# Kernel tuning notes

Measured on AMD Instinct MI355X. Metric: run time of the kernel, lower is better.

The kernel has to match this reference:

```python
import jax, jax.numpy as jnp
import numpy as np

N_NODES = 50000
N_EDGES = 800000
IN_F = 256
HID = 128
OUT_F = 128
HEADS = 4
NEG_SLOPE = 0.2


def setup_inputs() -> dict:
    key = jax.random.key(0)
    ks = jax.random.split(key, 10)
    x = jax.random.normal(ks[0], (N_NODES, IN_F), dtype=jnp.float32)
    edge_index = jax.random.randint(ks[1], (2, N_EDGES), 0, N_NODES, dtype=jnp.int64)
    # layer 1: in=256 -> heads=4, ch=128
    W1 = jax.random.normal(ks[2], (HEADS * HID, IN_F), dtype=jnp.float32) / np.sqrt(IN_F)
    att_src1 = jax.random.normal(ks[3], (HEADS, HID), dtype=jnp.float32) / np.sqrt(HID)
    att_dst1 = jax.random.normal(ks[4], (HEADS, HID), dtype=jnp.float32) / np.sqrt(HID)
    b1 = jnp.zeros((HID,), dtype=jnp.float32)
    # layer 2: in=128 -> heads=4, ch=128
    W2 = jax.random.normal(ks[5], (HEADS * OUT_F, HID), dtype=jnp.float32) / np.sqrt(HID)
    att_src2 = jax.random.normal(ks[6], (HEADS, OUT_F), dtype=jnp.float32) / np.sqrt(OUT_F)
    att_dst2 = jax.random.normal(ks[7], (HEADS, OUT_F), dtype=jnp.float32) / np.sqrt(OUT_F)
    b2 = jnp.zeros((OUT_F,), dtype=jnp.float32)
    return {"x": x, "edge_index": edge_index,
            "W1": W1, "att_src1": att_src1, "att_dst1": att_dst1, "b1": b1,
            "W2": W2, "att_src2": att_src2, "att_dst2": att_dst2, "b2": b2}


def gat_conv(x, src, dst, W, att_src, att_dst, b, heads, ch):
    n = x.shape[0]
    xh = (x @ W.T).reshape(n, heads, ch)                 # [N,H,C]
    a_s = jnp.einsum('nhc,hc->nh', xh, att_src)          # [N,H]
    a_d = jnp.einsum('nhc,hc->nh', xh, att_dst)
    alpha = a_s[src] + a_d[dst]                          # [E,H]
    alpha = jnp.where(alpha >= 0, alpha, NEG_SLOPE * alpha)
    # segment softmax over destination nodes
    amax = jax.ops.segment_max(alpha, dst, num_segments=n)
    amax = jnp.where(jnp.isfinite(amax), amax, 0.0)
    e = jnp.exp(alpha - amax[dst])                       # [E,H]
    denom = jax.ops.segment_sum(e, dst, num_segments=n)  # [N,H]
    coef = e / (denom[dst] + 1e-16)                      # [E,H]
    msg = xh[src] * coef[:, :, None]                     # [E,H,C]
    out = jax.ops.segment_sum(msg, dst, num_segments=n)  # [N,H,C]
    return out.mean(axis=1) + b                          # concat=False -> mean over heads


def reference(x, edge_index, W1, att_src1, att_dst1, b1, W2, att_src2, att_dst2, b2):
    n = x.shape[0]
    loops = jnp.arange(n, dtype=edge_index.dtype)
    src = jnp.concatenate([edge_index[0], loops])        # add_self_loops=True (PyG default)
    dst = jnp.concatenate([edge_index[1], loops])
    h = gat_conv(x, src, dst, W1, att_src1, att_dst1, b1, HEADS, HID)
    return gat_conv(h, src, dst, W2, att_src2, att_dst2, b2, HEADS, OUT_F)
```

## Files before the change

kernel.cpp:

```cpp
#include <hip/hip_runtime.h>
#include <hip/hip_fp16.h>
#include <math.h>

#define N_NODES 50000
#define MPAD    50176
#define N_EDGES 800000
#define E_TOT   (N_EDGES + N_NODES)
#define EB      ((E_TOT + 255) / 256)
#define HEADS   4
#define NEG_SLOPE 0.2f
#define SBLK    ((N_NODES + 255) / 256)

typedef unsigned int u32;
typedef unsigned short u16;
typedef __attribute__((ext_vector_type(8))) _Float16 f16x8;
typedef __attribute__((ext_vector_type(4))) float f32x4;



__global__ __launch_bounds__(256) void prep(const int* __restrict__ ei,
                                            int* __restrict__ deg,
                                            int* __restrict__ epos,
                                            const float* __restrict__ W1,
                                            __half* __restrict__ B1,
                                            const float* __restrict__ W2,
                                            __half* __restrict__ B2,
                                            const float* __restrict__ att_s1,
                                            const float* __restrict__ att_d1,
                                            const float* __restrict__ att_s2,
                                            const float* __restrict__ att_d2,
                                            float* __restrict__ ws1,
                                            float* __restrict__ wd1,
                                            float* __restrict__ ws2,
                                            float* __restrict__ wd2) {
  int b = blockIdx.x, tid = threadIdx.x;
  if (b < EB) {
    int e = b * 256 + tid;
    if (e < E_TOT) {
      int dst = (e < N_EDGES) ? ei[N_EDGES + e] : (e - N_EDGES);
      epos[e] = atomicAdd(&deg[dst], 1);
    }
    return;
  }
  if (b < EB + 128) {
    int k4 = (b - EB) * 256 + tid;
    float4 v = ((const float4*)W1)[k4];
    __half2 h01 = __float22half2_rn(make_float2(v.x, v.y));
    __half2 h23 = __float22half2_rn(make_float2(v.z, v.w));
    uint2 pk = make_uint2(*(u32*)&h01, *(u32*)&h23);
    int r = k4 >> 6, h = r >> 7, j = r & 127;
    ((uint2*)B1)[j * 256 + h * 64 + (k4 & 63)] = pk;
    return;
  }
  if (b < EB + 192) {
    int k4 = (b - EB - 128) * 256 + tid;
    float4 v = ((const float4*)W2)[k4];
    __half2 h01 = __float22half2_rn(make_float2(v.x, v.y));
    __half2 h23 = __float22half2_rn(make_float2(v.z, v.w));
    uint2 pk = make_uint2(*(u32*)&h01, *(u32*)&h23);
    int r = k4 >> 5, h = r >> 7, j = r & 127;
    ((uint2*)B2)[j * 128 + h * 32 + (k4 & 31)] = pk;
    return;
  }
  int bw = b - (EB + 192);
  int h = bw & 3;
  if (bw < 8) {
    const float* att = (bw < 4) ? att_s1 : att_d1;
    float* o = (bw < 4) ? ws1 : wd1;
    int k = tid;
    float acc = 0.f;
    for (int c = 0; c < 128; ++c)
      acc = fmaf(att[h * 128 + c], W1[(size_t)(h * 128 + c) * 256 + k], acc);
    o[h * 256 + k] = acc;
  } else {
    const float* att = (bw < 12) ? att_s2 : att_d2;
    float* o = (bw < 12) ? ws2 : wd2;
    if (tid < 128) {
      int k = tid;
      float acc = 0.f;
      for (int c = 0; c < 128; ++c)
        acc = fmaf(att[h * 128 + c], W2[(size_t)(h * 128 + c) * 128 + k], acc);
      o[h * 128 + k] = acc;
    }
  }
}


__global__ __launch_bounds__(256) void scan_blocks(const int* __restrict__ deg,
                                                   int* __restrict__ row_ptr,
                                                   int* __restrict__ bsum) {
  __shared__ int sh[256];
  int tid = threadIdx.x;
  int idx = blockIdx.x * 256 + tid;
  int v = (idx < N_NODES) ? deg[idx] : 0;
  sh[tid] = v;
  __syncthreads();
#pragma unroll
  for (int off = 1; off < 256; off <<= 1) {
    int t = (tid >= off) ? sh[tid - off] : 0;
    __syncthreads();
    sh[tid] += t;
    __syncthreads();
  }
  if (idx < N_NODES) row_ptr[idx + 1] = sh[tid];
  if (tid == 255) bsum[blockIdx.x] = sh[255];
}

__global__ __launch_bounds__(256) void scan_tops(int* __restrict__ bsum) {
  __shared__ int sh[256];
  int tid = threadIdx.x;
  int v = (tid < SBLK) ? bsum[tid] : 0;
  sh[tid] = v;
  __syncthreads();
#pragma unroll
  for (int off = 1; off < 256; off <<= 1) {
    int t = (tid >= off) ? sh[tid - off] : 0;
    __syncthreads();
    sh[tid] += t;
    __syncthreads();
  }
  if (tid < SBLK) bsum[tid] = sh[tid] - v;
}

__global__ __launch_bounds__(256) void scan_add(const int* __restrict__ bsum,
                                                int* __restrict__ row_ptr) {
  int idx = blockIdx.x * 256 + threadIdx.x;
  int off = bsum[blockIdx.x];
  if (idx < N_NODES) row_ptr[idx + 1] += off;
  if (idx == 0) row_ptr[0] = 0;
}

__device__ __forceinline__ float leaky_exp(float a) {
  a = (a >= 0.f) ? a : NEG_SLOPE * a;
  return __expf(a);
}


__global__ __launch_bounds__(256) void scatter_pos(const int* __restrict__ ei,
                                                   const int* __restrict__ epos,
                                                   const int* __restrict__ row_ptr,
                                                   int2* __restrict__ col2) {
  int e = blockIdx.x * 256 + threadIdx.x;
  if (e >= E_TOT) return;
  int src, dst;
  if (e < N_EDGES) { src = ei[e]; dst = ei[N_EDGES + e]; }
  else             { src = e - N_EDGES; dst = src; }
  int slot = row_ptr[dst] + epos[e];
  col2[slot] = make_int2(src, dst);
}


__global__ __launch_bounds__(256) void edge_weights(const int2* __restrict__ col2,
                                                    const float* __restrict__ as_,
                                                    const float* __restrict__ ad_,
                                                    float4* __restrict__ wtab) {
  int i = blockIdx.x * 256 + threadIdx.x;
  if (i >= E_TOT) return;
  int2 sd = col2[i];
  float4 a = ((const float4*)as_)[sd.x];
  float4 d = ((const float4*)ad_)[sd.y];
  float4 w;
  w.x = leaky_exp(a.x + d.x);
  w.y = leaky_exp(a.y + d.y);
  w.z = leaky_exp(a.z + d.z);
  w.w = leaky_exp(a.w + d.w);
  wtab[i] = w;
}


__global__ __launch_bounds__(256) void prep_x(const float* __restrict__ x,
                                              const float* __restrict__ ws1,
                                              const float* __restrict__ wd1,
                                              __half* __restrict__ x16,
                                              float* __restrict__ as_,
                                              float* __restrict__ ad_) {
  int node = (blockIdx.x * 256 + threadIdx.x) >> 6;
  if (node >= N_NODES) return;
  int lane = threadIdx.x & 63;
  int c4 = lane * 4;
  f32x4 xv = *(const f32x4*)(x + (size_t)node * 256 + c4);
  __half2 h01 = __float22half2_rn(make_float2(xv[0], xv[1]));
  __half2 h23 = __float22half2_rn(make_float2(xv[2], xv[3]));
  uint2 pk = make_uint2(*(u32*)&h01, *(u32*)&h23);
  *(uint2*)(x16 + (size_t)node * 256 + c4) = pk;
  float p[8];
#pragma unroll
  for (int v = 0; v < 4; ++v) {
    f32x4 w = *(const f32x4*)(ws1 + v * 256 + c4);
    p[v] = xv[0] * w[0] + xv[1] * w[1] + xv[2] * w[2] + xv[3] * w[3];
    f32x4 u = *(const f32x4*)(wd1 + v * 256 + c4);
    p[4 + v] = xv[0] * u[0] + xv[1] * u[1] + xv[2] * u[2] + xv[3] * u[3];
  }
#pragma unroll
  for (int k = 0; k < 8; ++k)
#pragma unroll
    for (int m = 1; m < 64; m <<= 1)
      p[k] += __shfl_xor(p[k], m, 64);
  if (lane == 0) {
    *(float4*)(as_ + (size_t)node * 4) = make_float4(p[0], p[1], p[2], p[3]);
    *(float4*)(ad_ + (size_t)node * 4) = make_float4(p[4], p[5], p[6], p[7]);
  }
}


__global__ __launch_bounds__(256) void score2(const __half* __restrict__ hrow,
                                              const float* __restrict__ ws2,
                                              const float* __restrict__ wd2,
                                              float* __restrict__ as_,
                                              float* __restrict__ ad_) {
  int node = (blockIdx.x * 256 + threadIdx.x) >> 6;
  if (node >= N_NODES) return;
  int lane = threadIdx.x & 63, c = lane * 2;
  float2 f = __half22float2(*(const __half2*)(hrow + (size_t)node * 128 + c));
  float p[8];
#pragma unroll
  for (int v = 0; v < 4; ++v) {
    float2 w = *(const float2*)(ws2 + v * 128 + c);
    p[v] = f.x * w.x + f.y * w.y;
    float2 u = *(const float2*)(wd2 + v * 128 + c);
    p[4 + v] = f.x * u.x + f.y * u.y;
  }
#pragma unroll
  for (int k = 0; k < 8; ++k)
#pragma unroll
    for (int m = 1; m < 64; m <<= 1)
      p[k] += __shfl_xor(p[k], m, 64);
  if (lane == 0) {
    *(float4*)(as_ + (size_t)node * 4) = make_float4(p[0], p[1], p[2], p[3]);
    *(float4*)(ad_ + (size_t)node * 4) = make_float4(p[4], p[5], p[6], p[7]);
  }
}


template <int CPL>
__global__ __launch_bounds__(256) void gat_aggregate_w(
    const __half* __restrict__ tbl, const float4* __restrict__ wtab,
    const int* __restrict__ row_ptr, const int2* __restrict__ col2,
    __half* __restrict__ agg) {
  constexpr int CHIN = CPL * 64;
  const int* colx = (const int*)col2;
  int node = (blockIdx.x * 256 + threadIdx.x) >> 6;
  if (node >= N_NODES) return;
  int lane = threadIdx.x & 63, cb = lane * CPL;
  const __half* tb = tbl + cb;
  int s = __builtin_amdgcn_readfirstlane(row_ptr[node]);
  int e = __builtin_amdgcn_readfirstlane(row_ptr[node + 1]);

  float acc[4][CPL];
#pragma unroll
  for (int h = 0; h < 4; ++h)
#pragma unroll
    for (int c = 0; c < CPL; ++c) acc[h][c] = 0.f;
  float den[4] = {0.f, 0.f, 0.f, 0.f};

  auto accum = [&](uint2 q, float4 w) {
    float wv[4] = {w.x, w.y, w.z, w.w};
#pragma unroll
    for (int h = 0; h < 4; ++h) den[h] += wv[h];
    float f[CPL];
    float2 f0 = __half22float2(*(__half2*)&q.x);
    f[0] = f0.x; f[1] = f0.y;
    if (CPL == 4) {
      float2 f1 = __half22float2(*(__half2*)&q.y);
      f[2] = f1.x; f[3] = f1.y;
    }
#pragma unroll
    for (int h = 0; h < 4; ++h)
#pragma unroll
      for (int c = 0; c < CPL; ++c)
        acc[h][c] = fmaf(wv[h], f[c], acc[h][c]);
  };
  auto loadq = [&](int src) -> uint2 {
    if (CPL == 4) return *(const uint2*)(tb + (size_t)src * CHIN);
    uint2 r; r.x = *(const u32*)(tb + (size_t)src * CHIN); r.y = 0;
    return r;
  };

  int i = s;
  for (; i + 4 <= e; i += 4) {
    int s0 = __builtin_amdgcn_readfirstlane(colx[2 * i]);
    int s1 = __builtin_amdgcn_readfirstlane(colx[2 * i + 2]);
    int s2 = __builtin_amdgcn_readfirstlane(colx[2 * i + 4]);
    int s3 = __builtin_amdgcn_readfirstlane(colx[2 * i + 6]);
    float4 w0 = wtab[i],     w1 = wtab[i + 1];
    float4 w2 = wtab[i + 2], w3 = wtab[i + 3];
    uint2 q0 = loadq(s0), q1 = loadq(s1), q2 = loadq(s2), q3 = loadq(s3);
    accum(q0, w0); accum(q1, w1); accum(q2, w2); accum(q3, w3);
  }
  for (; i < e; ++i) {
    int s0 = __builtin_amdgcn_readfirstlane(colx[2 * i]);
    float4 w0 = wtab[i];
    accum(loadq(s0), w0);
  }

#pragma unroll
  for (int h = 0; h < 4; ++h) {
    float inv = 1.f / (den[h] + 1e-16f);
    if (CPL == 4) {
      __half2 o0 = __float22half2_rn(make_float2(acc[h][0] * inv, acc[h][1] * inv));
      __half2 o1 = __float22half2_rn(make_float2(acc[h][2] * inv, acc[h][3] * inv));
      *(uint2*)(agg + (size_t)node * 4 * CHIN + h * CHIN + cb) =
          make_uint2(*(u32*)&o0, *(u32*)&o1);
    } else {
      __half2 o0 = __float22half2_rn(make_float2(acc[h][0] * inv, acc[h][1] * inv));
      *(u32*)(agg + (size_t)node * 4 * CHIN + h * CHIN + cb) = *(u32*)&o0;
    }
  }
}


#define GLD16(gp, lp)                                                          \
  __builtin_amdgcn_global_load_lds(                                            \
      (const __attribute__((address_space(1))) u32*)(gp),                      \
      (__attribute__((address_space(3))) u32*)(lp), 16, 0, 0)

template <int K, bool HALF_OUT>
__global__ __launch_bounds__(256, 4) void gemm_mean(
    const __half* __restrict__ A, const __half* __restrict__ Bm,
    const float* __restrict__ bias, void* __restrict__ outv) {
  __shared__ u16 sA[64 * 32];
  __shared__ u16 sB[128 * 32];
  const int tid = threadIdx.x, lane = tid & 63, wave = tid >> 6;
  const int m0 = blockIdx.x * 64;
  const int wm = (wave >> 1) * 32, wn = (wave & 1) * 64;
  const int t = lane & 15, quad = lane >> 4;

  f32x4 acc[2][4];
#pragma unroll
  for (int i = 0; i < 2; i++)
#pragma unroll
    for (int j = 0; j < 4; j++) acc[i][j] = (f32x4){0.f, 0.f, 0.f, 0.f};

  const char* gpA; u32 offA;
  {
    int row = tid >> 2, w16 = tid & 3;
    gpA = (const char*)A + ((size_t)(m0 + row) * K) * 2 + w16 * 16;
    offA = (u32)tid * 16;
  }
  const char* gpB[2]; u32 offB[2];
#pragma unroll
  for (int r = 0; r < 2; ++r) {
    int c = tid + r * 256;
    int row = c >> 2, w16 = c & 3;
    gpB[r] = (const char*)Bm + ((size_t)row * K) * 2 + w16 * 16;
    offB[r] = (u32)c * 16;
  }

  for (int k0 = 0; k0 < K; k0 += 32) {
    __syncthreads();
    GLD16(gpA, (char*)sA + offA); gpA += 64;
#pragma unroll
    for (int r = 0; r < 2; ++r) { GLD16(gpB[r], (char*)sB + offB[r]); gpB[r] += 64; }
    __syncthreads();

    f16x8 a[2], b[4];
#pragma unroll
    for (int i = 0; i < 2; ++i)
      a[i] = *(const f16x8*)&sA[(wm + t + i * 16) * 32 + quad * 8];
#pragma unroll
    for (int j = 0; j < 4; ++j)
      b[j] = *(const f16x8*)&sB[(wn + t + j * 16) * 32 + quad * 8];
#pragma unroll
    for (int i = 0; i < 2; ++i)
#pragma unroll
      for (int j = 0; j < 4; ++j)
        acc[i][j] = __builtin_amdgcn_mfma_f32_16x16x32_f16(a[i], b[j], acc[i][j], 0, 0, 0);
  }

  float bv[4];
#pragma unroll
  for (int j = 0; j < 4; ++j) bv[j] = bias[wn + j * 16 + t];
#pragma unroll
  for (int i = 0; i < 2; ++i)
#pragma unroll
    for (int j = 0; j < 4; ++j)
#pragma unroll
      for (int r = 0; r < 4; ++r) {
        int m = m0 + wm + i * 16 + quad * 4 + r;
        if (m < N_NODES) {
          int n = wn + j * 16 + t;
          float v = 0.25f * acc[i][j][r] + bv[j];
          if (HALF_OUT) ((__half*)outv)[(size_t)m * 128 + n] = __float2half(v);
          else          ((float*)outv)[(size_t)m * 128 + n] = v;
        }
      }
}


extern "C" void kernel_launch(void* const* d_in, const int* in_sizes, int n_in,
                              void* d_out, int out_size, void* d_ws, size_t ws_size,
                              hipStream_t stream) {
  const float* x      = (const float*)d_in[0];
  const int*   ei     = (const int*)  d_in[1];
  const float* W1     = (const float*)d_in[2];
  const float* att_s1 = (const float*)d_in[3];
  const float* att_d1 = (const float*)d_in[4];
  const float* b1     = (const float*)d_in[5];
  const float* W2     = (const float*)d_in[6];
  const float* att_s2 = (const float*)d_in[7];
  const float* att_d2 = (const float*)d_in[8];
  const float* b2     = (const float*)d_in[9];
  float* out = (float*)d_out;

  char* ws = (char*)d_ws;
  size_t off = 0;
  auto alloc = [&](size_t bytes) -> void* {
    void* p = ws + off;
    off += (bytes + 255) & ~(size_t)255;
    return p;
  };
  __half* x16  = (__half*)alloc((size_t)MPAD * 256 * 2);
  __half* agg1 = (__half*)alloc((size_t)MPAD * 1024 * 2);
  __half* B1p  = (__half*)alloc((size_t)128 * 1024 * 2);
  __half* B2p  = (__half*)alloc((size_t)128 * 512 * 2);
  float* ws1 = (float*)alloc(4 * 256 * 4);
  float* wd1 = (float*)alloc(4 * 256 * 4);
  float* ws2 = (float*)alloc(4 * 128 * 4);
  float* wd2 = (float*)alloc(4 * 128 * 4);
  float* as1 = (float*)alloc((size_t)N_NODES * 4 * 4);
  float* ad1 = (float*)alloc((size_t)N_NODES * 4 * 4);
  float* as2 = (float*)alloc((size_t)N_NODES * 4 * 4);
  float* ad2 = (float*)alloc((size_t)N_NODES * 4 * 4);
  int*   row_ptr = (int*)alloc((size_t)(N_NODES + 1) * 4);
  int*   deg     = (int*)alloc((size_t)N_NODES * 4);
  int*   bsum    = (int*)alloc((size_t)256 * 4);
  int*   epos    = (int*)alloc((size_t)E_TOT * 4);
  int2*  col2    = (int2*)alloc((size_t)E_TOT * 8);
  float4* wtab   = (float4*)alloc((size_t)E_TOT * 16);

  __half* out1 = x16;
  __half* agg2 = agg1;

  const int edge_blocks = (E_TOT + 255) / 256;
  const int node_wave_blocks = (N_NODES + 3) / 4;

  hipMemsetAsync(deg, 0, (size_t)N_NODES * 4, stream);
  prep<<<EB + 208, 256, 0, stream>>>(ei, deg, epos, W1, B1p, W2, B2p,
                                     att_s1, att_d1, att_s2, att_d2,
                                     ws1, wd1, ws2, wd2);
  scan_blocks<<<SBLK, 256, 0, stream>>>(deg, row_ptr, bsum);
  scan_tops<<<1, 256, 0, stream>>>(bsum);
  scan_add<<<SBLK, 256, 0, stream>>>(bsum, row_ptr);
  scatter_pos<<<edge_blocks, 256, 0, stream>>>(ei, epos, row_ptr, col2);

  prep_x<<<node_wave_blocks, 256, 0, stream>>>(x, ws1, wd1, x16, as1, ad1);
  edge_weights<<<edge_blocks, 256, 0, stream>>>(col2, as1, ad1, wtab);
  gat_aggregate_w<4><<<node_wave_blocks, 256, 0, stream>>>(
      x16, wtab, row_ptr, col2, agg1);
  gemm_mean<1024, true><<<MPAD / 64, 256, 0, stream>>>(agg1, B1p, b1, out1);

  score2<<<node_wave_blocks, 256, 0, stream>>>(out1, ws2, wd2, as2, ad2);
  edge_weights<<<edge_blocks, 256, 0, stream>>>(col2, as2, ad2, wtab);
  gat_aggregate_w<2><<<node_wave_blocks, 256, 0, stream>>>(
      out1, wtab, row_ptr, col2, agg2);
  gemm_mean<512, false><<<MPAD / 64, 256, 0, stream>>>(agg2, B2p, b2, out);
}
```

Before: 391.6 us.

## Fuse layer-2 score computation into GEMM epilogue and fold scan offsets into consumers

Removes the score2 kernel by computing the layer-2 attention source/destination scores inside the first GEMM's epilogue, using shuffles and shared memory to reduce across columns and waves. It also drops the scan_add kernel: scatter_pos and the aggregate kernels now add the per-block prefix offset from bsum themselves. This saves two launches and one reread of the hidden features, at the cost of extra epilogue work and registers in the GEMM and extra bsum loads in the consumers.

```diff
diff --git a/kernel.cpp b/kernel.cpp
--- a/kernel.cpp
+++ b/kernel.cpp
@@ -122,14 +122,6 @@
   if (tid < SBLK) bsum[tid] = sh[tid] - v;
 }
 
-__global__ __launch_bounds__(256) void scan_add(const int* __restrict__ bsum,
-                                                int* __restrict__ row_ptr) {
-  int idx = blockIdx.x * 256 + threadIdx.x;
-  int off = bsum[blockIdx.x];
-  if (idx < N_NODES) row_ptr[idx + 1] += off;
-  if (idx == 0) row_ptr[0] = 0;
-}
-
 __device__ __forceinline__ float leaky_exp(float a) {
   a = (a >= 0.f) ? a : NEG_SLOPE * a;
   return __expf(a);
@@ -139,13 +131,15 @@
 __global__ __launch_bounds__(256) void scatter_pos(const int* __restrict__ ei,
                                                    const int* __restrict__ epos,
                                                    const int* __restrict__ row_ptr,
+                                                   const int* __restrict__ bsum,
                                                    int2* __restrict__ col2) {
   int e = blockIdx.x * 256 + threadIdx.x;
   if (e >= E_TOT) return;
   int src, dst;
   if (e < N_EDGES) { src = ei[e]; dst = ei[N_EDGES + e]; }
   else             { src = e - N_EDGES; dst = src; }
-  int slot = row_ptr[dst] + epos[e];
+  int rp = (dst == 0) ? 0 : (row_ptr[dst] + bsum[(dst - 1) >> 8]);
+  int slot = rp + epos[e];
   col2[slot] = make_int2(src, dst);
 }
 
@@ -203,48 +197,22 @@
 }
 
 
-__global__ __launch_bounds__(256) void score2(const __half* __restrict__ hrow,
-                                              const float* __restrict__ ws2,
-                                              const float* __restrict__ wd2,
-                                              float* __restrict__ as_,
-                                              float* __restrict__ ad_) {
-  int node = (blockIdx.x * 256 + threadIdx.x) >> 6;
-  if (node >= N_NODES) return;
-  int lane = threadIdx.x & 63, c = lane * 2;
-  float2 f = __half22float2(*(const __half2*)(hrow + (size_t)node * 128 + c));
-  float p[8];
-#pragma unroll
-  for (int v = 0; v < 4; ++v) {
-    float2 w = *(const float2*)(ws2 + v * 128 + c);
-    p[v] = f.x * w.x + f.y * w.y;
-    float2 u = *(const float2*)(wd2 + v * 128 + c);
-    p[4 + v] = f.x * u.x + f.y * u.y;
-  }
-#pragma unroll
-  for (int k = 0; k < 8; ++k)
-#pragma unroll
-    for (int m = 1; m < 64; m <<= 1)
-      p[k] += __shfl_xor(p[k], m, 64);
-  if (lane == 0) {
-    *(float4*)(as_ + (size_t)node * 4) = make_float4(p[0], p[1], p[2], p[3]);
-    *(float4*)(ad_ + (size_t)node * 4) = make_float4(p[4], p[5], p[6], p[7]);
-  }
-}
-
-
 template <int CPL>
 __global__ __launch_bounds__(256) void gat_aggregate_w(
     const __half* __restrict__ tbl, const float4* __restrict__ wtab,
-    const int* __restrict__ row_ptr, const int2* __restrict__ col2,
-    __half* __restrict__ agg) {
+    const int* __restrict__ row_ptr, const int* __restrict__ bsum,
+    const int2* __restrict__ col2, __half* __restrict__ agg) {
   constexpr int CHIN = CPL * 64;
   const int* colx = (const int*)col2;
   int node = (blockIdx.x * 256 + threadIdx.x) >> 6;
   if (node >= N_NODES) return;
   int lane = threadIdx.x & 63, cb = lane * CPL;
   const __half* tb = tbl + cb;
-  int s = __builtin_amdgcn_readfirstlane(row_ptr[node]);
-  int e = __builtin_amdgcn_readfirstlane(row_ptr[node + 1]);
+  int s = (node == 0)
+              ? 0
+              : __builtin_amdgcn_readfirstlane(row_ptr[node] +
+                                               bsum[(node - 1) >> 8]);
+  int e = __builtin_amdgcn_readfirstlane(row_ptr[node + 1] + bsum[node >> 8]);
 
   float acc[4][CPL];
 #pragma unroll
@@ -314,12 +282,16 @@
       (const __attribute__((address_space(1))) u32*)(gp),                      \
       (__attribute__((address_space(3))) u32*)(lp), 16, 0, 0)
 
-template <int K, bool HALF_OUT>
+template <int K, bool HALF_OUT, bool SCORES>
 __global__ __launch_bounds__(256, 4) void gemm_mean(
     const __half* __restrict__ A, const __half* __restrict__ Bm,
-    const float* __restrict__ bias, void* __restrict__ outv) {
+    const float* __restrict__ bias, void* __restrict__ outv,
+    const float* __restrict__ ws2, const float* __restrict__ wd2,
+    float* __restrict__ as2g, float* __restrict__ ad2g) {
   __shared__ u16 sA[64 * 32];
   __shared__ u16 sB[128 * 32];
+  __shared__ float sS[2][64][4];
+  __shared__ float sD[2][64][4];
   const int tid = threadIdx.x, lane = tid & 63, wave = tid >> 6;
   const int m0 = blockIdx.x * 64;
   const int wm = (wave >> 1) * 32, wn = (wave & 1) * 64;
@@ -370,20 +342,72 @@
   float bv[4];
 #pragma unroll
   for (int j = 0; j < 4; ++j) bv[j] = bias[wn + j * 16 + t];
+
+  float ws2v[4][4], wd2v[4][4];
+  if constexpr (SCORES) {
+#pragma unroll
+    for (int h = 0; h < 4; ++h)
+#pragma unroll
+      for (int j = 0; j < 4; ++j) {
+        int n = wn + j * 16 + t;
+        ws2v[h][j] = ws2[h * 128 + n];
+        wd2v[h][j] = wd2[h * 128 + n];
+      }
+  }
+
 #pragma unroll
   for (int i = 0; i < 2; ++i)
 #pragma unroll
-    for (int j = 0; j < 4; ++j)
-#pragma unroll
-      for (int r = 0; r < 4; ++r) {
-        int m = m0 + wm + i * 16 + quad * 4 + r;
+    for (int r = 0; r < 4; ++r) {
+      int m = m0 + wm + i * 16 + quad * 4 + r;
+      float vj[4];
+#pragma unroll
+      for (int j = 0; j < 4; ++j) {
+        float v = 0.25f * acc[i][j][r] + bv[j];
+        __half hv = __float2half(v);
+        vj[j] = __half2float(hv);
         if (m < N_NODES) {
           int n = wn + j * 16 + t;
-          float v = 0.25f * acc[i][j][r] + bv[j];
-          if (HALF_OUT) ((__half*)outv)[(size_t)m * 128 + n] = __float2half(v);
+          if (HALF_OUT) ((__half*)outv)[(size_t)m * 128 + n] = hv;
           else          ((float*)outv)[(size_t)m * 128 + n] = v;
         }
       }
+      if constexpr (SCORES) {
+        float ps[4], pd[4];
+#pragma unroll
+        for (int h = 0; h < 4; ++h) {
+          ps[h] = vj[0] * ws2v[h][0] + vj[1] * ws2v[h][1] +
+                  vj[2] * ws2v[h][2] + vj[3] * ws2v[h][3];
+          pd[h] = vj[0] * wd2v[h][0] + vj[1] * wd2v[h][1] +
+                  vj[2] * wd2v[h][2] + vj[3] * wd2v[h][3];
+        }
+#pragma unroll
+        for (int mask = 1; mask < 16; mask <<= 1)
+#pragma unroll
+          for (int h = 0; h < 4; ++h) {
+            ps[h] += __shfl_xor(ps[h], mask, 64);
+            pd[h] += __shfl_xor(pd[h], mask, 64);
+          }
+        if (t == 0) {
+          int rl = wm + i * 16 + quad * 4 + r;
+#pragma unroll
+          for (int h = 0; h < 4; ++h) {
+            sS[wave & 1][rl][h] = ps[h];
+            sD[wave & 1][rl][h] = pd[h];
+          }
+        }
+      }
+    }
+
+  if constexpr (SCORES) {
+    __syncthreads();
+    int row = tid >> 2, h = tid & 3;
+    int gm = m0 + row;
+    if (gm < N_NODES) {
+      as2g[gm * 4 + h] = sS[0][row][h] + sS[1][row][h];
+      ad2g[gm * 4 + h] = sD[0][row][h] + sD[1][row][h];
+    }
+  }
 }
 
 
@@ -440,18 +464,18 @@
                                      ws1, wd1, ws2, wd2);
   scan_blocks<<<SBLK, 256, 0, stream>>>(deg, row_ptr, bsum);
   scan_tops<<<1, 256, 0, stream>>>(bsum);
-  scan_add<<<SBLK, 256, 0, stream>>>(bsum, row_ptr);
-  scatter_pos<<<edge_blocks, 256, 0, stream>>>(ei, epos, row_ptr, col2);
+  scatter_pos<<<edge_blocks, 256, 0, stream>>>(ei, epos, row_ptr, bsum, col2);
 
   prep_x<<<node_wave_blocks, 256, 0, stream>>>(x, ws1, wd1, x16, as1, ad1);
   edge_weights<<<edge_blocks, 256, 0, stream>>>(col2, as1, ad1, wtab);
   gat_aggregate_w<4><<<node_wave_blocks, 256, 0, stream>>>(
-      x16, wtab, row_ptr, col2, agg1);
-  gemm_mean<1024, true><<<MPAD / 64, 256, 0, stream>>>(agg1, B1p, b1, out1);
-
-  score2<<<node_wave_blocks, 256, 0, stream>>>(out1, ws2, wd2, as2, ad2);
+      x16, wtab, row_ptr, bsum, col2, agg1);
+  gemm_mean<1024, true, true><<<MPAD / 64, 256, 0, stream>>>(
+      agg1, B1p, b1, out1, ws2, wd2, as2, ad2);
+
   edge_weights<<<edge_blocks, 256, 0, stream>>>(col2, as2, ad2, wtab);
   gat_aggregate_w<2><<<node_wave_blocks, 256, 0, stream>>>(
-      out1, wtab, row_ptr, col2, agg2);
-  gemm_mean<512, false><<<MPAD / 64, 256, 0, stream>>>(agg2, B2p, b2, out);
-}
+      out1, wtab, row_ptr, bsum, col2, agg2);
+  gemm_mean<512, false, false><<<MPAD / 64, 256, 0, stream>>>(
+      agg2, B2p, b2, out, nullptr, nullptr, nullptr, nullptr);
+}
```

New measurement: 386.2 us. No clear change (-1.4%).
